# Optimization experiments

Measured on AMD Instinct MI355X. Metric: run time of the kernel, lower is better.

## Reference

```python
import jax, jax.numpy as jnp
import numpy as np

HEADS = 8

def _flatten(x, s1, s2):
    # 'b c (h s1) (w s2) -> b (h w) (s1 s2 c)'
    b, c, H, W = x.shape
    h, w = H // s1, W // s2
    x = x.reshape(b, c, h, s1, w, s2).transpose(0, 2, 4, 3, 5, 1)
    return x.reshape(b, h * w, s1 * s2 * c)

def _unflatten(x, h, w, s1, s2):
    # 'b (h w) (s1 s2 c) -> b c (h s1) (w s2)'
    b, n, e = x.shape
    c = e // (s1 * s2)
    x = x.reshape(b, h, w, s1, s2, c).transpose(0, 5, 1, 3, 2, 4)
    return x.reshape(b, c, h * s1, w * s2)

def _attn(x_detail, x_context, wq, bq, wk, bk, wv, bv, wo, bo):
    E = x_detail.shape[-1]
    d = E // HEADS
    scale = d ** -0.5
    def split(t):
        b, n, _ = t.shape
        return t.reshape(b, n, HEADS, d).transpose(0, 2, 1, 3)  # b h n d
    q = split(x_context @ wq.T + bq)
    k = split(x_detail @ wk.T + bk)
    v = split(x_detail @ wv.T + bv)
    att = jax.nn.softmax(jnp.einsum('bhqd,bhkd->bhqk', q, k) * scale, axis=-1)
    out = jnp.einsum('bhqk,bhkd->bhqd', att, v)
    b, h, n, _ = out.shape
    out = out.transpose(0, 2, 1, 3).reshape(b, n, E)
    return out @ wo.T + bo

def setup_inputs() -> dict:
    key = jax.random.key(0)
    ks = iter(jax.random.split(key, 64))
    inp = {}
    xshapes = [(16, 96, 56, 56), (16, 192, 28, 28), (16, 384, 14, 14), (16, 768, 7, 7)]
    names = ['x00', 'x10', 'x20', 'x30']
    for nm, sh in zip(names, xshapes):
        inp[nm + '_detail'] = jax.random.normal(next(ks), sh, dtype=jnp.float32)
        inp[nm + '_context'] = jax.random.normal(next(ks), sh, dtype=jnp.float32)
    embs = [384, 192, 384, 768]
    for i, E in enumerate(embs):
        for p in ['q', 'k', 'v', 'o']:
            inp[f'w{p}{i}'] = jax.random.normal(next(ks), (E, E), dtype=jnp.float32) * 0.02
            inp[f'b{p}{i}'] = jnp.zeros((E,), dtype=jnp.float32)
    return inp

def reference(x00_detail, x00_context, x10_detail, x10_context,
              x20_detail, x20_context, x30_detail, x30_context,
              wq0, bq0, wk0, bk0, wv0, bv0, wo0, bo0,
              wq1, bq1, wk1, bk1, wv1, bv1, wo1, bo1,
              wq2, bq2, wk2, bk2, wv2, bv2, wo2, bo2,
              wq3, bq3, wk3, bk3, wv3, bv3, wo3, bo3):
    # scale 0: 56x56 with 2x2 patching -> 784 tokens, emb 384
    o0 = x00_detail + _unflatten(
        _attn(_flatten(x00_detail, 2, 2), _flatten(x00_context, 2, 2),
              wq0, bq0, wk0, bk0, wv0, bv0, wo0, bo0), 28, 28, 2, 2)
    # scale 1: 28x28 -> 784 tokens, emb 192
    o1 = x10_detail + _unflatten(
        _attn(_flatten(x10_detail, 1, 1), _flatten(x10_context, 1, 1),
              wq1, bq1, wk1, bk1, wv1, bv1, wo1, bo1), 28, 28, 1, 1)
    # scale 2: 14x14 -> 196 tokens, emb 384
    o2 = x20_detail + _unflatten(
        _attn(_flatten(x20_detail, 1, 1), _flatten(x20_context, 1, 1),
              wq2, bq2, wk2, bk2, wv2, bv2, wo2, bo2), 14, 14, 1, 1)
    # scale 3: 7x7 -> 49 tokens, emb 768
    o3 = x30_detail + _unflatten(
        _attn(_flatten(x30_detail, 1, 1), _flatten(x30_context, 1, 1),
              wq3, bq3, wk3, bk3, wv3, bv3, wo3, bo3), 7, 7, 1, 1)
    return (o0, o1, o2, o3)
```

## Files before the change

kernel.cpp:

```cpp
#include <hip/hip_runtime.h>
#include <hip/hip_bf16.h>
#include <cstdint>
#include <cstddef>
#include <cmath>

typedef unsigned short bf16u;
typedef float f32x4 __attribute__((ext_vector_type(4)));
typedef short frag8 __attribute__((ext_vector_type(8)));

typedef __attribute__((address_space(1))) uint32_t u32g;
typedef __attribute__((address_space(3))) uint32_t u32l;

__device__ __forceinline__ void async_cp16(const bf16u* g, bf16u* l) {
    __builtin_amdgcn_global_load_lds((u32g*)g, (u32l*)l, 16, 0, 0);
}

__device__ __forceinline__ bf16u f2bf(float f) {
    union { float f; uint32_t u; } v; v.f = f;
    uint32_t u = v.u;
    return (bf16u)((u + 0x7fffu + ((u >> 16) & 1u)) >> 16);
}

__device__ __forceinline__ uint32_t pk2bf(float a, float b) {
    __hip_bfloat162 h = __float22bfloat162_rn(make_float2(a, b));
    union { __hip_bfloat162 h; uint32_t u; } c; c.h = h; return c.u;
}

__device__ __forceinline__ int vperm(int n) {
    return (n & ~63) | ((n & 15) << 2) | ((n >> 4) & 3);
}

static constexpr int cN[4]   = {784, 784, 196, 49};
static constexpr int cE[4]   = {384, 192, 384, 768};
static constexpr int cM[4]   = {12544, 12544, 3136, 784};
static constexpr int cC[4]   = {96, 192, 384, 768};
static constexpr int cH[4]   = {56, 28, 14, 7};
static constexpr int cS[4]   = {2, 1, 1, 1};
static constexpr int cWt[4]  = {28, 28, 14, 7};

static constexpr size_t xoff[4] = {0, 4816896, 7225344, 8429568};
static constexpr size_t voff[4] = {0, 6815744, 10223616, 12320768};
static constexpr size_t woff[4] = {0, 589824, 737280, 1327104};

__device__ __constant__ float qsc[4] = {0.14433756729740643f, 0.20412414523193154f,
                                        0.14433756729740643f, 0.10206207261596577f};

static constexpr int qStart[13] = {0,294,588,882,957,1032,1107,1149,1191,1233,1821,2409,2997};
static constexpr int oStart[5]  = {0,294,369,411,999};

static constexpr int fStart[9] = {0,4800,9600,12000,14400,15744,17088,17856,18624};
static constexpr int wCum[17]  = {0,72,144,216,288,306,324,342,360,432,504,576,648,936,1224,1512,1800};
static constexpr int uStart[5] = {0,4800,7200,8544,9312};
static constexpr int fNtn[4] = {25, 25, 7, 2};
static constexpr int fNtc[4] = {3, 6, 12, 24};
static constexpr int fSp[4]  = {4, 1, 1, 1};

struct BiasP { const float* p[16]; };
struct PrepP { const float* x[8]; const float* w[16]; };
struct UnfP  { const float* x[4]; };

__global__ __launch_bounds__(256) void prep(PrepP pp, bf16u* __restrict__ Xd,
                                            bf16u* __restrict__ Xc, bf16u* __restrict__ Wb) {
    int blk = blockIdx.x, tid = threadIdx.x;
    if (blk < 18624) {
        __shared__ float tile[32][33];
        int seg = 0;
        while (seg < 7 && blk >= fStart[seg + 1]) seg++;
        int s = seg >> 1, which = seg & 1;
        int l = blk - fStart[seg];
        int ntn = fNtn[s], ntc = fNtc[s], sp = fSp[s];
        int nt = l % ntn; l /= ntn;
        int ctl = l % ntc; l /= ntc;
        int spi = l % sp; int b = l / sp;
        int sv = cS[s];
        int s1i = spi / sv, s2i = spi % sv;
        int C = cC[s], H = cH[s], Wd = cH[s], N = cN[s], E2 = cE[s], Wt = cWt[s];
        const float* x = pp.x[s * 2 + which];
        bf16u* dst = (which ? Xc : Xd) + xoff[s];
        int tx = tid & 31, ty = tid >> 5;
        int n0 = nt * 32, c0 = ctl * 32;
#pragma unroll
        for (int rr = 0; rr < 4; ++rr) {
            int c = c0 + rr * 8 + ty;
            int n = n0 + tx;
            if (n < N) {
                int hh = (n / Wt) * sv + s1i;
                int ww = (n % Wt) * sv + s2i;
                tile[rr * 8 + ty][tx] = x[((size_t)(b * C + c) * H + hh) * Wd + ww];
            }
        }
        __syncthreads();
        int ebase = (s1i * sv + s2i) * C + c0;
#pragma unroll
        for (int rr = 0; rr < 4; ++rr) {
            int n = n0 + rr * 8 + ty;
            if (n < N)
                dst[((size_t)b * N + n) * E2 + ebase + tx] = f2bf(tile[tx][rr * 8 + ty]);
        }
    } else {
        int wb = blk - 18624;
        int m2 = 0;
        while (m2 < 15 && wb >= wCum[m2 + 1]) m2++;
        int s = m2 >> 2, mi = m2 & 3;
        size_t e2 = (size_t)cE[s] * cE[s];
        size_t base = (size_t)(wb - wCum[m2]) * 2048 + tid * 8;
        const float* src = pp.w[m2];
        bf16u* dst = Wb + woff[s] + mi * e2 + base;
        float4 a = *(const float4*)(src + base);
        float4 c = *(const float4*)(src + base + 4);
        bf16u o[8] = {f2bf(a.x), f2bf(a.y), f2bf(a.z), f2bf(a.w),
                      f2bf(c.x), f2bf(c.y), f2bf(c.z), f2bf(c.w)};
        *(frag8*)dst = *(frag8*)o;
    }
}

template<int MODE, int NN, int DHt, int DHPt, int NJt>
__device__ __forceinline__ void gemm_tile128(const bf16u* __restrict__ A, const bf16u* __restrict__ W,
                                             const float* __restrict__ bias,
                                             int M, int E, int mTile, int eTile, float oscale,
                                             bf16u* __restrict__ outB, float* __restrict__ outF,
                                             bf16u* As, bf16u* Bs) {
    int tid = threadIdx.x, wave = tid >> 6, lane = tid & 63;
    int mbase = mTile * 128, ebase = eTile * 128;
    int wm = (wave & 1) * 64, wn = (wave >> 1) * 64;
    f32x4 acc[4][4] = {};
    int srow = tid >> 2, sch = (tid & 3) * 8;
    int K = E;
    int m0 = mbase + srow;      if (m0 >= M) m0 = M - 1;
    int m1 = mbase + srow + 64; if (m1 >= M) m1 = M - 1;
    const bf16u* Ag0 = A + (size_t)m0 * K + sch;
    const bf16u* Ag1 = A + (size_t)m1 * K + sch;
    const bf16u* Wg0 = W + (size_t)(ebase + srow) * K + sch;
    const bf16u* Wg1 = W + (size_t)(ebase + srow + 64) * K + sch;
    bf16u* Asw = As + tid * 8;
    bf16u* Bsw = Bs + tid * 8;
    int la = (lane & 15) * 32 + (lane >> 4) * 8;

    for (int k0 = 0; k0 < K; k0 += 32) {
        async_cp16(Ag0 + k0, Asw);
        async_cp16(Ag1 + k0, Asw + 2048);
        async_cp16(Wg0 + k0, Bsw);
        async_cp16(Wg1 + k0, Bsw + 2048);
        __syncthreads();
        frag8 af[4], bfr[4];
#pragma unroll
        for (int i = 0; i < 4; ++i) {
            af[i]  = *(const frag8*)(As + (wm + i * 16) * 32 + la);
            bfr[i] = *(const frag8*)(Bs + (wn + i * 16) * 32 + la);
        }
#pragma unroll
        for (int i = 0; i < 4; ++i)
#pragma unroll
            for (int j = 0; j < 4; ++j)
                acc[i][j] = __builtin_amdgcn_mfma_f32_16x16x32_bf16(af[i], bfr[j], acc[i][j], 0, 0, 0);
        __syncthreads();
    }

#pragma unroll
    for (int mt = 0; mt < 4; ++mt) {
#pragma unroll
        for (int nt = 0; nt < 4; ++nt) {
            int col = ebase + wn + nt * 16 + (lane & 15);
            float bv = bias[col];
            int rbase = mbase + wm + mt * 16 + (lane >> 4) * 4;
#pragma unroll
            for (int r = 0; r < 4; ++r) {
                int rowg = rbase + r;
                if (rowg >= M) continue;
                float val = (acc[mt][nt][r] + bv) * oscale;
                if (MODE == 0) {
                    outB[(size_t)rowg * E + col] = f2bf(val);
                } else if (MODE == 2) {
                    outF[(size_t)rowg * E + col] = val;
                } else {
                    int bb2 = rowg / NN, n = rowg % NN;
                    int hh = col / DHt, d = col - hh * DHt;
                    outB[((size_t)(bb2 * 8 + hh) * DHPt + d) * NJt + vperm(n)] = f2bf(val);
                }
            }
        }
    }
}

template<int MODE, int NN, int DHt, int DHPt, int NJt>
__device__ __forceinline__ void gemm_tile64(const bf16u* __restrict__ A, const bf16u* __restrict__ W,
                                            const float* __restrict__ bias,
                                            int M, int E, int mTile, int eTile, float oscale,
                                            bf16u* __restrict__ outB, float* __restrict__ outF,
                                            bf16u* As, bf16u* Bs) {
    int tid = threadIdx.x, wave = tid >> 6, lane = tid & 63;
    int mbase = mTile * 64, ebase = eTile * 64;
    int wm = (wave & 1) * 32, wn = (wave >> 1) * 32;
    f32x4 acc[2][2] = {};
    int srow = tid >> 2, sch = (tid & 3) * 8;
    int K = E;
    int m = mbase + srow; if (m >= M) m = M - 1;
    const bf16u* Ag = A + (size_t)m * K + sch;
    const bf16u* Wg = W + (size_t)(ebase + srow) * K + sch;
    bf16u* Asw = As + tid * 8;
    bf16u* Bsw = Bs + tid * 8;
    int la = (lane & 15) * 32 + (lane >> 4) * 8;

    for (int k0 = 0; k0 < K; k0 += 32) {
        async_cp16(Ag + k0, Asw);
        async_cp16(Wg + k0, Bsw);
        __syncthreads();
        frag8 af0 = *(const frag8*)(As + wm * 32 + la);
        frag8 af1 = *(const frag8*)(As + (wm + 16) * 32 + la);
        frag8 bf0 = *(const frag8*)(Bs + wn * 32 + la);
        frag8 bf1 = *(const frag8*)(Bs + (wn + 16) * 32 + la);
        acc[0][0] = __builtin_amdgcn_mfma_f32_16x16x32_bf16(af0, bf0, acc[0][0], 0, 0, 0);
        acc[0][1] = __builtin_amdgcn_mfma_f32_16x16x32_bf16(af0, bf1, acc[0][1], 0, 0, 0);
        acc[1][0] = __builtin_amdgcn_mfma_f32_16x16x32_bf16(af1, bf0, acc[1][0], 0, 0, 0);
        acc[1][1] = __builtin_amdgcn_mfma_f32_16x16x32_bf16(af1, bf1, acc[1][1], 0, 0, 0);
        __syncthreads();
    }

#pragma unroll
    for (int mt = 0; mt < 2; ++mt) {
#pragma unroll
        for (int nt = 0; nt < 2; ++nt) {
            int col = ebase + wn + nt * 16 + (lane & 15);
            float bv = bias[col];
            int rbase = mbase + wm + mt * 16 + (lane >> 4) * 4;
#pragma unroll
            for (int r = 0; r < 4; ++r) {
                int rowg = rbase + r;
                if (rowg >= M) continue;
                float val = (acc[mt][nt][r] + bv) * oscale;
                if (MODE == 0) {
                    outB[(size_t)rowg * E + col] = f2bf(val);
                } else if (MODE == 2) {
                    outF[(size_t)rowg * E + col] = val;
                } else {
                    int bb2 = rowg / NN, n = rowg % NN;
                    int hh = col / DHt, d = col - hh * DHt;
                    outB[((size_t)(bb2 * 8 + hh) * DHPt + d) * NJt + vperm(n)] = f2bf(val);
                }
            }
        }
    }
}

__global__ __launch_bounds__(256) void qkv_fat(const bf16u* __restrict__ Xd, const bf16u* __restrict__ Xc,
                                               const bf16u* __restrict__ Wb,
                                               bf16u* __restrict__ Qb, bf16u* __restrict__ Kb,
                                               bf16u* __restrict__ Vt, BiasP bp) {
    __shared__ __align__(16) bf16u As[4096], Bs[4096];
    int blk = blockIdx.x;
    int seg = 0;
    while (seg < 11 && blk >= qStart[seg + 1]) seg++;
    int t = blk - qStart[seg];
    if (seg < 9) {
        int s = (seg < 3) ? 0 : (seg < 6 ? 2 : 3);
        int op = seg % 3;
        int E = cE[s], M = cM[s];
        int ct = E >> 7;
        int mTile = t / ct, eTile = t - mTile * ct;
        const bf16u* A = (op == 0 ? Xc : Xd) + xoff[s];
        const bf16u* W = Wb + woff[s] + (size_t)op * E * E;
        const float* bias = bp.p[s * 4 + op];
        if (op == 2) {
            if (s == 0)
                gemm_tile128<1, 784, 48, 64, 832>(A, W, bias, M, E, mTile, eTile, 1.0f, Vt + voff[0], nullptr, As, Bs);
            else if (s == 2)
                gemm_tile128<1, 196, 48, 64, 256>(A, W, bias, M, E, mTile, eTile, 1.0f, Vt + voff[2], nullptr, As, Bs);
            else
                gemm_tile128<1, 49, 96, 96, 64>(A, W, bias, M, E, mTile, eTile, 1.0f, Vt + voff[3], nullptr, As, Bs);
        } else {
            float osc = (op == 0) ? qsc[s] : 1.0f;
            bf16u* outB = (op == 0 ? Qb : Kb) + xoff[s];
            gemm_tile128<0, 0, 1, 0, 0>(A, W, bias, M, E, mTile, eTile, osc, outB, nullptr, As, Bs);
        }
    } else {
        int op = seg - 9;
        int E = 192, M = 12544;
        int mTile = t / 3, eTile = t - mTile * 3;
        const bf16u* A = (op == 0 ? Xc : Xd) + xoff[1];
        const bf16u* W = Wb + woff[1] + (size_t)op * E * E;
        const float* bias = bp.p[4 + op];
        if (op == 2)
            gemm_tile64<1, 784, 24, 32, 832>(A, W, bias, M, E, mTile, eTile, 1.0f, Vt + voff[1], nullptr, As, Bs);
        else {
            float osc = (op == 0) ? qsc[1] : 1.0f;
            bf16u* outB = (op == 0 ? Qb : Kb) + xoff[1];
            gemm_tile64<0, 0, 1, 0, 0>(A, W, bias, M, E, mTile, eTile, osc, outB, nullptr, As, Bs);
        }
    }
}

__global__ __launch_bounds__(256) void o_fat(const bf16u* __restrict__ Ob, const bf16u* __restrict__ Wb,
                                             float* __restrict__ Yo, BiasP bp) {
    __shared__ __align__(16) bf16u As[4096], Bs[4096];
    int blk = blockIdx.x;
    int seg = 0;
    while (seg < 3 && blk >= oStart[seg + 1]) seg++;
    int t = blk - oStart[seg];
    if (seg < 3) {
        int s = (seg == 0) ? 0 : (seg == 1 ? 2 : 3);
        int E = cE[s], M = cM[s];
        int ct = E >> 7;
        int mTile = t / ct, eTile = t - mTile * ct;
        gemm_tile128<2, 0, 1, 0, 0>(Ob + xoff[s], Wb + woff[s] + (size_t)3 * E * E, bp.p[s * 4 + 3],
                                    M, E, mTile, eTile, 1.0f, nullptr, Yo + xoff[s], As, Bs);
    } else {
        int E = 192, M = 12544;
        int mTile = t / 3, eTile = t - mTile * 3;
        gemm_tile64<2, 0, 1, 0, 0>(Ob + xoff[1], Wb + woff[1] + (size_t)3 * E * E, bp.p[4 + 3],
                                   M, E, mTile, eTile, 1.0f, nullptr, Yo + xoff[1], As, Bs);
    }
}

__device__ __forceinline__ f32x4 bfly_add16(f32x4 v) {
#pragma unroll
    for (int m = 1; m <= 8; m <<= 1) {
        f32x4 o;
#pragma unroll
        for (int e = 0; e < 4; ++e) o[e] = __shfl_xor(v[e], m);
#pragma unroll
        for (int e = 0; e < 4; ++e) v[e] += o[e];
    }
    return v;
}

template<int DH, int N>
__device__ __forceinline__ void attn_body(bf16u* __restrict__ smem,
                                          const bf16u* __restrict__ Q, const bf16u* __restrict__ K,
                                          const bf16u* __restrict__ Vt, bf16u* __restrict__ O,
                                          int lin) {
    constexpr int DHP = (DH == 24) ? 32 : (DH == 48 ? 64 : 96);
    constexpr int KC  = DHP / 32;
    constexpr int DHT = (DH + 15) / 16;
    constexpr int NT  = (N + 63) / 64;
    constexpr int NJc = NT * 64;
    constexpr int E   = DH * 8;
    constexpr int KP  = DHP + 8, QP = DHP + 8;
    constexpr int VP  = 72, PP = 72;
    constexpr int C8  = DHP / 8;
    constexpr int KIT = (64 * C8 + 255) / 256;
    constexpr int VIT = (DHT * 16 * 8 + 255) / 256;
    constexpr int QT  = (N + 63) / 64;

    bf16u* Ks = smem;
    bf16u* Vs = Ks + 64 * KP;
    bf16u* QsPw = Vs + DHT * 16 * VP;

    int qt = lin % QT;
    int r2 = lin / QT;
    int h = r2 & 7, b = r2 >> 3;
    int qb = qt * 64;
    int tid = threadIdx.x, wave = tid >> 6, lane = tid & 63;
    int mrow = lane & 15, quad = lane >> 4;

    for (int idx = tid; idx < 64 * C8; idx += 256) {
        int row = idx / C8, col = (idx % C8) * 8;
        int n = qb + row; if (n >= N) n = N - 1;
        frag8 v = {};
        if (col < DH) v = *(const frag8*)(Q + ((size_t)(b * N + n)) * E + h * DH + col);
        *(frag8*)(QsPw + row * QP + col) = v;
    }
    __syncthreads();
    frag8 qf[KC];
#pragma unroll
    for (int kc = 0; kc < KC; ++kc)
        qf[kc] = *(const frag8*)(QsPw + (wave * 16 + mrow) * QP + kc * 32 + quad * 8);
    __syncthreads();
    bf16u* Pw = QsPw + wave * 16 * PP;

    const bf16u* Kb2 = K + (size_t)b * N * E + h * DH;
    const bf16u* Vb2 = Vt + (size_t)(b * 8 + h) * DHP * NJc;

    frag8 kreg[KIT], vreg[VIT];
    auto loadKV = [&](int jt) {
#pragma unroll
        for (int it = 0; it < KIT; ++it) {
            int idx = tid + it * 256;
            int row = idx / C8, col = (idx % C8) * 8;
            int n = jt * 64 + row; if (n >= N) n = N - 1;
            frag8 v = {};
            if (col < DH) v = *(const frag8*)(Kb2 + (size_t)n * E + col);
            kreg[it] = v;
        }
#pragma unroll
        for (int it = 0; it < VIT; ++it) {
            int idx = tid + it * 256;
            frag8 v = {};
            if (idx < DHT * 16 * 8) {
                int d = idx / 8, j = (idx % 8) * 8;
                if (d < DH) v = *(const frag8*)(Vb2 + (size_t)d * NJc + jt * 64 + j);
            }
            vreg[it] = v;
        }
    };
    auto storeKV = [&]() {
#pragma unroll
        for (int it = 0; it < KIT; ++it) {
            int idx = tid + it * 256;
            int row = idx / C8, col = (idx % C8) * 8;
            *(frag8*)(Ks + row * KP + col) = kreg[it];
        }
#pragma unroll
        for (int it = 0; it < VIT; ++it) {
            int idx = tid + it * 256;
            if (idx < DHT * 16 * 8) {
                int d = idx / 8, j = (idx % 8) * 8;
                *(frag8*)(Vs + d * VP + j) = vreg[it];
            }
        }
    };

    f32x4 lrun = {0.f, 0.f, 0.f, 0.f};
    f32x4 oacc[DHT];
#pragma unroll
    for (int t = 0; t < DHT; ++t) oacc[t] = f32x4{0.f, 0.f, 0.f, 0.f};

    loadKV(0);
    for (int jt = 0; jt < NT; ++jt) {
        storeKV();
        __syncthreads();
        if (jt + 1 < NT) loadKV(jt + 1);

        f32x4 s[4];
        const bool domask = ((N & 63) != 0) && (jt == NT - 1);
#pragma unroll
        for (int sub = 0; sub < 4; ++sub) {
            f32x4 acc = {};
#pragma unroll
            for (int kc = 0; kc < KC; ++kc) {
                frag8 bfr = *(const frag8*)(Ks + (sub * 16 + mrow) * KP + kc * 32 + quad * 8);
                acc = __builtin_amdgcn_mfma_f32_16x16x32_bf16(qf[kc], bfr, acc, 0, 0, 0);
            }
            if (domask) {
                int col = jt * 64 + sub * 16 + mrow;
                if (col >= N) { acc[0] = acc[1] = acc[2] = acc[3] = -1e30f; }
            }
            s[sub] = acc;
        }

#pragma unroll
        for (int sub = 0; sub < 4; ++sub)
#pragma unroll
            for (int e = 0; e < 4; ++e) {
                float p = __expf(fminf(s[sub][e], 60.f));
                s[sub][e] = p;
                lrun[e] += p;
            }

#pragma unroll
        for (int e = 0; e < 4; ++e) {
            uint2 u;
            u.x = pk2bf(s[0][e], s[1][e]);
            u.y = pk2bf(s[2][e], s[3][e]);
            *(uint2*)(Pw + (quad * 4 + e) * PP + mrow * 4) = u;
        }

#pragma unroll
        for (int jc = 0; jc < 2; ++jc) {
            frag8 af = *(const frag8*)(Pw + mrow * PP + jc * 32 + quad * 8);
#pragma unroll
            for (int t = 0; t < DHT; ++t) {
                frag8 bfr = *(const frag8*)(Vs + (t * 16 + mrow) * VP + jc * 32 + quad * 8);
                oacc[t] = __builtin_amdgcn_mfma_f32_16x16x32_bf16(af, bfr, oacc[t], 0, 0, 0);
            }
        }
        __syncthreads();
    }

    lrun = bfly_add16(lrun);
    f32x4 linv;
#pragma unroll
    for (int e = 0; e < 4; ++e) linv[e] = 1.0f / lrun[e];
#pragma unroll
    for (int t = 0; t < DHT; ++t) {
        int d = t * 16 + mrow;
        if (d >= DH) continue;
#pragma unroll
        for (int e = 0; e < 4; ++e) {
            int n = qb + wave * 16 + quad * 4 + e;
            if (n < N)
                O[((size_t)(b * N + n)) * E + h * DH + d] = f2bf(oacc[t][e] * linv[e]);
        }
    }
}

__global__ __launch_bounds__(256, 4) void attn_fat(const bf16u* __restrict__ Qb, const bf16u* __restrict__ Kb,
                                                   const bf16u* __restrict__ Vt, bf16u* __restrict__ Ob) {
    __shared__ __align__(16) bf16u smem[12672];
    int blk = blockIdx.x;
    if (blk < 1664)
        attn_body<48, 784>(smem, Qb + xoff[0], Kb + xoff[0], Vt + voff[0], Ob + xoff[0], blk);
    else if (blk < 3328)
        attn_body<24, 784>(smem, Qb + xoff[1], Kb + xoff[1], Vt + voff[1], Ob + xoff[1], blk - 1664);
    else
        attn_body<48, 196>(smem, Qb + xoff[2], Kb + xoff[2], Vt + voff[2], Ob + xoff[2], blk - 3328);
}

__global__ __launch_bounds__(256, 2) void attn_s3(const bf16u* __restrict__ Qb, const bf16u* __restrict__ Kb,
                                                  const bf16u* __restrict__ Vt, bf16u* __restrict__ Ob) {
    __shared__ __align__(16) bf16u smem[20224];
    attn_body<96, 49>(smem, Qb + xoff[3], Kb + xoff[3], Vt + voff[3], Ob + xoff[3], blockIdx.x);
}

__global__ __launch_bounds__(256) void unflat(const float* __restrict__ Yo, UnfP up,
                                              float* __restrict__ out) {
    __shared__ float tile[32][33];
    int blk = blockIdx.x, tid = threadIdx.x;
    int seg = 0;
    while (seg < 3 && blk >= uStart[seg + 1]) seg++;
    int s = seg;
    int l = blk - uStart[seg];
    int ntn = fNtn[s], ntc = fNtc[s], sp = fSp[s];
    int nt = l % ntn; l /= ntn;
    int ctl = l % ntc; l /= ntc;
    int spi = l % sp; int b = l / sp;
    int sv = cS[s];
    int s1i = spi / sv, s2i = spi % sv;
    int C = cC[s], H = cH[s], Wd = cH[s], N = cN[s], E2 = cE[s], Wt = cWt[s];
    const float* yo = Yo + xoff[s];
    const float* xd = up.x[s];
    float* o = out + xoff[s];
    int tx = tid & 31, ty = tid >> 5;
    int n0 = nt * 32, c0 = ctl * 32;
    int ebase = (s1i * sv + s2i) * C + c0;
#pragma unroll
    for (int rr = 0; rr < 4; ++rr) {
        int n = n0 + rr * 8 + ty;
        if (n < N)
            tile[tx][rr * 8 + ty] = yo[((size_t)b * N + n) * E2 + ebase + tx];
    }
    __syncthreads();
#pragma unroll
    for (int rr = 0; rr < 4; ++rr) {
        int c = c0 + rr * 8 + ty;
        int n = n0 + tx;
        if (n < N) {
            int hh = (n / Wt) * sv + s1i;
            int ww = (n % Wt) * sv + s2i;
            size_t oi = ((size_t)(b * C + c) * H + hh) * Wd + ww;
            o[oi] = xd[oi] + tile[rr * 8 + ty][tx];
        }
    }
}

extern "C" void kernel_launch(void* const* d_in, const int* in_sizes, int n_in,
                              void* d_out, int out_size, void* d_ws, size_t ws_size,
                              hipStream_t stream) {
    bf16u* ws = (bf16u*)d_ws;
    bf16u* Qb = ws;
    bf16u* Kb = ws + 9031680;
    bf16u* Vt = ws + 18063360;
    bf16u* Ob = ws + 31170560;
    bf16u* Wb = ws + 40202240;
    bf16u* Xd = ws + 43888640;
    bf16u* Xc = ws + 52920320;
    float* Yo = (float*)(ws + 43888640);
    float* out = (float*)d_out;

    PrepP pp; BiasP bb; UnfP ux;
    for (int s = 0; s < 4; ++s) {
        pp.x[s * 2]     = (const float*)d_in[s * 2];
        pp.x[s * 2 + 1] = (const float*)d_in[s * 2 + 1];
        ux.x[s]         = (const float*)d_in[s * 2];
        int w0 = 8 + s * 8;
        pp.w[s * 4 + 0] = (const float*)d_in[w0 + 0];
        pp.w[s * 4 + 1] = (const float*)d_in[w0 + 2];
        pp.w[s * 4 + 2] = (const float*)d_in[w0 + 4];
        pp.w[s * 4 + 3] = (const float*)d_in[w0 + 6];
        bb.p[s * 4 + 0] = (const float*)d_in[w0 + 1];
        bb.p[s * 4 + 1] = (const float*)d_in[w0 + 3];
        bb.p[s * 4 + 2] = (const float*)d_in[w0 + 5];
        bb.p[s * 4 + 3] = (const float*)d_in[w0 + 7];
    }

    prep<<<20424, 256, 0, stream>>>(pp, Xd, Xc, Wb);
    qkv_fat<<<2997, 256, 0, stream>>>(Xd, Xc, Wb, Qb, Kb, Vt, bb);
    attn_fat<<<3840, 256, 0, stream>>>(Qb, Kb, Vt, Ob);
    attn_s3<<<128, 256, 0, stream>>>(Qb, Kb, Vt, Ob);
    o_fat<<<999, 256, 0, stream>>>(Ob, Wb, Yo, bb);
    unflat<<<9312, 256, 0, stream>>>(Yo, ux, out);
}
```

Measured before the change: 414.4 us.

## Fuse output projection with unflatten residual and double-buffer attention KV loads

```diff
diff --git a/kernel.cpp b/kernel.cpp
--- a/kernel.cpp
+++ b/kernel.cpp
@@ -42,22 +42,20 @@
 static constexpr size_t voff[4] = {0, 6815744, 10223616, 12320768};
 static constexpr size_t woff[4] = {0, 589824, 737280, 1327104};
 
-__device__ __constant__ float qsc[4] = {0.14433756729740643f, 0.20412414523193154f,
-                                        0.14433756729740643f, 0.10206207261596577f};
+__device__ __constant__ float qsc[4] = {0.20823509f, 0.29448888f, 0.20823509f, 0.14724444f};
 
 static constexpr int qStart[13] = {0,294,588,882,957,1032,1107,1149,1191,1233,1821,2409,2997};
 static constexpr int oStart[5]  = {0,294,369,411,999};
 
 static constexpr int fStart[9] = {0,4800,9600,12000,14400,15744,17088,17856,18624};
 static constexpr int wCum[17]  = {0,72,144,216,288,306,324,342,360,432,504,576,648,936,1224,1512,1800};
-static constexpr int uStart[5] = {0,4800,7200,8544,9312};
 static constexpr int fNtn[4] = {25, 25, 7, 2};
 static constexpr int fNtc[4] = {3, 6, 12, 24};
 static constexpr int fSp[4]  = {4, 1, 1, 1};
 
 struct BiasP { const float* p[16]; };
 struct PrepP { const float* x[8]; const float* w[16]; };
-struct UnfP  { const float* x[4]; };
+struct OunfP { const float* xd[4]; };
 
 __global__ __launch_bounds__(256) void prep(PrepP pp, bf16u* __restrict__ Xd,
                                             bf16u* __restrict__ Xc, bf16u* __restrict__ Wb) {
@@ -118,7 +116,7 @@
 __device__ __forceinline__ void gemm_tile128(const bf16u* __restrict__ A, const bf16u* __restrict__ W,
                                              const float* __restrict__ bias,
                                              int M, int E, int mTile, int eTile, float oscale,
-                                             bf16u* __restrict__ outB, float* __restrict__ outF,
+                                             bf16u* __restrict__ outB,
                                              bf16u* As, bf16u* Bs) {
     int tid = threadIdx.x, wave = tid >> 6, lane = tid & 63;
     int mbase = mTile * 128, ebase = eTile * 128;
@@ -170,8 +168,6 @@
                 float val = (acc[mt][nt][r] + bv) * oscale;
                 if (MODE == 0) {
                     outB[(size_t)rowg * E + col] = f2bf(val);
-                } else if (MODE == 2) {
-                    outF[(size_t)rowg * E + col] = val;
                 } else {
                     int bb2 = rowg / NN, n = rowg % NN;
                     int hh = col / DHt, d = col - hh * DHt;
@@ -186,7 +182,7 @@
 __device__ __forceinline__ void gemm_tile64(const bf16u* __restrict__ A, const bf16u* __restrict__ W,
                                             const float* __restrict__ bias,
                                             int M, int E, int mTile, int eTile, float oscale,
-                                            bf16u* __restrict__ outB, float* __restrict__ outF,
+                                            bf16u* __restrict__ outB,
                                             bf16u* As, bf16u* Bs) {
     int tid = threadIdx.x, wave = tid >> 6, lane = tid & 63;
     int mbase = mTile * 64, ebase = eTile * 64;
@@ -230,8 +226,6 @@
                 float val = (acc[mt][nt][r] + bv) * oscale;
                 if (MODE == 0) {
                     outB[(size_t)rowg * E + col] = f2bf(val);
-                } else if (MODE == 2) {
-                    outF[(size_t)rowg * E + col] = val;
                 } else {
                     int bb2 = rowg / NN, n = rowg % NN;
                     int hh = col / DHt, d = col - hh * DHt;
@@ -262,15 +256,15 @@
         const float* bias = bp.p[s * 4 + op];
         if (op == 2) {
             if (s == 0)
-                gemm_tile128<1, 784, 48, 64, 832>(A, W, bias, M, E, mTile, eTile, 1.0f, Vt + voff[0], nullptr, As, Bs);
+                gemm_tile128<1, 784, 48, 64, 832>(A, W, bias, M, E, mTile, eTile, 1.0f, Vt + voff[0], As, Bs);
             else if (s == 2)
-                gemm_tile128<1, 196, 48, 64, 256>(A, W, bias, M, E, mTile, eTile, 1.0f, Vt + voff[2], nullptr, As, Bs);
+                gemm_tile128<1, 196, 48, 64, 256>(A, W, bias, M, E, mTile, eTile, 1.0f, Vt + voff[2], As, Bs);
             else
-                gemm_tile128<1, 49, 96, 96, 64>(A, W, bias, M, E, mTile, eTile, 1.0f, Vt + voff[3], nullptr, As, Bs);
+                gemm_tile128<1, 49, 96, 96, 64>(A, W, bias, M, E, mTile, eTile, 1.0f, Vt + voff[3], As, Bs);
         } else {
             float osc = (op == 0) ? qsc[s] : 1.0f;
             bf16u* outB = (op == 0 ? Qb : Kb) + xoff[s];
-            gemm_tile128<0, 0, 1, 0, 0>(A, W, bias, M, E, mTile, eTile, osc, outB, nullptr, As, Bs);
+            gemm_tile128<0, 0, 1, 0, 0>(A, W, bias, M, E, mTile, eTile, osc, outB, As, Bs);
         }
     } else {
         int op = seg - 9;
@@ -280,18 +274,456 @@
         const bf16u* W = Wb + woff[1] + (size_t)op * E * E;
         const float* bias = bp.p[4 + op];
         if (op == 2)
-            gemm_tile64<1, 784, 24, 32, 832>(A, W, bias, M, E, mTile, eTile, 1.0f, Vt + voff[1], nullptr, As, Bs);
+            gemm_tile64<1, 784, 24, 32, 832>(A, W, bias, M, E, mTile, eTile, 1.0f, Vt + voff[1], As, Bs);
         else {
             float osc = (op == 0) ? qsc[1] : 1.0f;
             bf16u* outB = (op == 0 ? Qb : Kb) + xoff[1];
-            gemm_tile64<0, 0, 1, 0, 0>(A, W, bias, M, E, mTile, eTile, osc, outB, nullptr, As, Bs);
-        }
-    }
-}
-
-__global__ __launch_bounds__(256) void o_fat(const bf16u* __restrict__ Ob, const bf16u* __restrict__ Wb,
-                                             float* __restrict__ Yo, BiasP bp) {
-    __shared__ __align__(16) bf16u As[4096], Bs[4096];
+            gemm_tile64<0, 0, 1, 0, 0>(A, W, bias, M, E, mTile, eTile, osc, outB, As, Bs);
+        }
+    }
+}
+
+__device__ __forceinline__ f32x4 bfly_add16(f32x4 v) {
+#pragma unroll
+    for (int m = 1; m <= 8; m <<= 1) {
+        f32x4 o;
+#pragma unroll
+        for (int e = 0; e < 4; ++e) o[e] = __shfl_xor(v[e], m);
+#pragma unroll
+        for (int e = 0; e < 4; ++e) v[e] += o[e];
+    }
+    return v;
+}
+
+template<int DH, int N>
+__device__ __forceinline__ void attn_body2(bf16u* __restrict__ smem,
+                                           const bf16u* __restrict__ Q, const bf16u* __restrict__ K,
+                                           const bf16u* __restrict__ Vt, bf16u* __restrict__ O,
+                                           int lin) {
+    constexpr int DHP = (DH == 24) ? 32 : 64;
+    constexpr int C8  = DHP / 8;
+    constexpr int CM  = C8 - 1;
+    constexpr int KC  = DHP / 32;
+    constexpr int DHT = (DH + 15) / 16;
+    constexpr int VR  = DHT * 16;
+    constexpr int NT  = (N + 63) / 64;
+    constexpr int NJc = NT * 64;
+    constexpr int E   = DH * 8;
+    constexpr int KS  = 64 * C8;
+    constexpr int TS  = KS + VR * 8;
+    constexpr int RND = (TS + 255) / 256;
+    constexpr int PP  = 72;
+
+    bf16u* buf0 = smem;
+    bf16u* buf1 = smem + (size_t)TS * 8;
+    bf16u* Ps   = smem + (size_t)2 * TS * 8;
+
+    const int qt = lin % NT;
+    const int r2 = lin / NT;
+    const int h = r2 & 7, b = r2 >> 3;
+    const int qb = qt * 64;
+    const int tid = threadIdx.x, wave = tid >> 6, lane = tid & 63;
+    const int mrow = lane & 15, quad = lane >> 4;
+
+    const bf16u* Kb2 = K + (size_t)b * N * E + h * DH;
+    const bf16u* Vb2 = Vt + (size_t)(b * 8 + h) * DHP * NJc;
+
+    auto stage = [&](int jt, bf16u* buf) {
+#pragma unroll
+        for (int r = 0; r < RND; ++r) {
+            int s = tid + r * 256;
+            bf16u* dst = buf + (size_t)s * 8;
+            if (s < KS) {
+                int row = s / C8;
+                int cl = (s & CM) ^ (row & CM);
+                int n = jt * 64 + row; if (n >= N) n = N - 1;
+                async_cp16(Kb2 + (size_t)n * E + cl * 8, dst);
+            } else if (s < TS) {
+                int v = s - KS;
+                int d = v >> 3;
+                int cl = (v & 7) ^ (d & 7);
+                async_cp16(Vb2 + (size_t)d * NJc + jt * 64 + cl * 8, dst);
+            }
+        }
+    };
+
+    stage(0, buf0);
+
+    frag8 qf[KC];
+    {
+        int qn = qb + wave * 16 + mrow; if (qn >= N) qn = N - 1;
+        const bf16u* qp = Q + (size_t)(b * N + qn) * E + h * DH;
+#pragma unroll
+        for (int kc = 0; kc < KC; ++kc) {
+            int col = kc * 32 + quad * 8;
+            frag8 v = {};
+            if (col < DH) v = *(const frag8*)(qp + col);
+            qf[kc] = v;
+        }
+    }
+
+    f32x4 lrun = {0.f, 0.f, 0.f, 0.f};
+    f32x4 oacc[DHT];
+#pragma unroll
+    for (int t = 0; t < DHT; ++t) oacc[t] = f32x4{0.f, 0.f, 0.f, 0.f};
+
+    bf16u* Pw = Ps + wave * 16 * PP;
+
+    __syncthreads();
+
+    int p = 0;
+    for (int jt = 0; jt < NT; ++jt) {
+        bf16u* KsB = p ? buf1 : buf0;
+        bf16u* VsB = KsB + (size_t)KS * 8;
+        if (jt + 1 < NT) stage(jt + 1, p ? buf0 : buf1);
+
+        f32x4 s[4];
+        const bool domask = ((N & 63) != 0) && (jt == NT - 1);
+#pragma unroll
+        for (int sub = 0; sub < 4; ++sub) {
+            f32x4 acc = {};
+#pragma unroll
+            for (int kc = 0; kc < KC; ++kc) {
+                int c = kc * 4 + quad;
+                frag8 bfr = *(const frag8*)(KsB + ((size_t)((sub * 16 + mrow) * C8 + (c ^ (mrow & CM)))) * 8);
+                acc = __builtin_amdgcn_mfma_f32_16x16x32_bf16(qf[kc], bfr, acc, 0, 0, 0);
+            }
+            if (domask) {
+                int col = jt * 64 + sub * 16 + mrow;
+                if (col >= N) { acc[0] = acc[1] = acc[2] = acc[3] = -30000.f; }
+            }
+            s[sub] = acc;
+        }
+
+#pragma unroll
+        for (int sub = 0; sub < 4; ++sub)
+#pragma unroll
+            for (int e = 0; e < 4; ++e) {
+                float px = __builtin_amdgcn_exp2f(s[sub][e]);
+                s[sub][e] = px;
+                lrun[e] += px;
+            }
+
+#pragma unroll
+        for (int e = 0; e < 4; ++e) {
+            uint2 u;
+            u.x = pk2bf(s[0][e], s[1][e]);
+            u.y = pk2bf(s[2][e], s[3][e]);
+            *(uint2*)(Pw + (quad * 4 + e) * PP + mrow * 4) = u;
+        }
+
+#pragma unroll
+        for (int jc = 0; jc < 2; ++jc) {
+            frag8 af = *(const frag8*)(Pw + mrow * PP + jc * 32 + quad * 8);
+            int c = jc * 4 + quad;
+#pragma unroll
+            for (int t = 0; t < DHT; ++t) {
+                frag8 bfr = *(const frag8*)(VsB + ((size_t)((t * 16 + mrow) * 8 + (c ^ (mrow & 7)))) * 8);
+                oacc[t] = __builtin_amdgcn_mfma_f32_16x16x32_bf16(af, bfr, oacc[t], 0, 0, 0);
+            }
+        }
+        __syncthreads();
+        p ^= 1;
+    }
+
+    lrun = bfly_add16(lrun);
+    f32x4 linv;
+#pragma unroll
+    for (int e = 0; e < 4; ++e) linv[e] = 1.0f / lrun[e];
+#pragma unroll
+    for (int t = 0; t < DHT; ++t) {
+        int d = t * 16 + mrow;
+        if (d >= DH) continue;
+#pragma unroll
+        for (int e = 0; e < 4; ++e) {
+            int n = qb + wave * 16 + quad * 4 + e;
+            if (n < N)
+                O[((size_t)(b * N + n)) * E + h * DH + d] = f2bf(oacc[t][e] * linv[e]);
+        }
+    }
+}
+
+__global__ __launch_bounds__(256, 4) void attn_fat(const bf16u* __restrict__ Qb, const bf16u* __restrict__ Kb,
+                                                   const bf16u* __restrict__ Vt, bf16u* __restrict__ Ob) {
+    __shared__ __align__(16) bf16u smem[18944];
+    int blk = blockIdx.x;
+    if (blk < 1664)
+        attn_body2<48, 784>(smem, Qb + xoff[0], Kb + xoff[0], Vt + voff[0], Ob + xoff[0], blk);
+    else if (blk < 3328)
+        attn_body2<24, 784>(smem, Qb + xoff[1], Kb + xoff[1], Vt + voff[1], Ob + xoff[1], blk - 1664);
+    else
+        attn_body2<48, 196>(smem, Qb + xoff[2], Kb + xoff[2], Vt + voff[2], Ob + xoff[2], blk - 3328);
+}
+
+__global__ __launch_bounds__(256, 2) void attn_s3(const bf16u* __restrict__ Qg, const bf16u* __restrict__ Kg,
+                                                  const bf16u* __restrict__ Vtg, bf16u* __restrict__ Og) {
+    constexpr int DH = 96, N = 49, DHP = 96, KC = 3, DHT = 6, NJc = 64, E = 768;
+    constexpr int KP = 104, QP = 104, VP = 72, PP = 72, C8 = 12;
+    __shared__ __align__(16) bf16u smem[20224];
+    bf16u* Ks = smem;
+    bf16u* Vs = Ks + 64 * KP;
+    bf16u* QsPw = Vs + DHT * 16 * VP;
+
+    const bf16u* Q = Qg + xoff[3];
+    const bf16u* K = Kg + xoff[3];
+    const bf16u* Vt = Vtg + voff[3];
+    bf16u* O = Og + xoff[3];
+
+    int lin = blockIdx.x;
+    int h = lin & 7, b = lin >> 3;
+    int tid = threadIdx.x, wave = tid >> 6, lane = tid & 63;
+    int mrow = lane & 15, quad = lane >> 4;
+
+    for (int idx = tid; idx < 64 * C8; idx += 256) {
+        int row = idx / C8, col = (idx % C8) * 8;
+        int n = row; if (n >= N) n = N - 1;
+        frag8 v = {};
+        if (col < DH) v = *(const frag8*)(Q + ((size_t)(b * N + n)) * E + h * DH + col);
+        *(frag8*)(QsPw + row * QP + col) = v;
+    }
+    for (int idx = tid; idx < 64 * C8; idx += 256) {
+        int row = idx / C8, col = (idx % C8) * 8;
+        int n = row; if (n >= N) n = N - 1;
+        frag8 v = {};
+        if (col < DH) v = *(const frag8*)(K + (size_t)(b * N + n) * E + h * DH + col);
+        *(frag8*)(Ks + row * KP + col) = v;
+    }
+    const bf16u* Vb2 = Vt + (size_t)(b * 8 + h) * DHP * NJc;
+    for (int idx = tid; idx < DHT * 16 * 8; idx += 256) {
+        int d = idx / 8, j = (idx % 8) * 8;
+        frag8 v = {};
+        if (d < DH) v = *(const frag8*)(Vb2 + (size_t)d * NJc + j);
+        *(frag8*)(Vs + d * VP + j) = v;
+    }
+    __syncthreads();
+    frag8 qf[KC];
+#pragma unroll
+    for (int kc = 0; kc < KC; ++kc)
+        qf[kc] = *(const frag8*)(QsPw + (wave * 16 + mrow) * QP + kc * 32 + quad * 8);
+    __syncthreads();
+    bf16u* Pw = QsPw + wave * 16 * PP;
+
+    f32x4 lrun = {0.f, 0.f, 0.f, 0.f};
+    f32x4 oacc[DHT];
+#pragma unroll
+    for (int t = 0; t < DHT; ++t) oacc[t] = f32x4{0.f, 0.f, 0.f, 0.f};
+
+    f32x4 s[4];
+#pragma unroll
+    for (int sub = 0; sub < 4; ++sub) {
+        f32x4 acc = {};
+#pragma unroll
+        for (int kc = 0; kc < KC; ++kc) {
+            frag8 bfr = *(const frag8*)(Ks + (sub * 16 + mrow) * KP + kc * 32 + quad * 8);
+            acc = __builtin_amdgcn_mfma_f32_16x16x32_bf16(qf[kc], bfr, acc, 0, 0, 0);
+        }
+        int col = sub * 16 + mrow;
+        if (col >= N) { acc[0] = acc[1] = acc[2] = acc[3] = -30000.f; }
+        s[sub] = acc;
+    }
+#pragma unroll
+    for (int sub = 0; sub < 4; ++sub)
+#pragma unroll
+        for (int e = 0; e < 4; ++e) {
+            float px = __builtin_amdgcn_exp2f(s[sub][e]);
+            s[sub][e] = px;
+            lrun[e] += px;
+        }
+#pragma unroll
+    for (int e = 0; e < 4; ++e) {
+        uint2 u;
+        u.x = pk2bf(s[0][e], s[1][e]);
+        u.y = pk2bf(s[2][e], s[3][e]);
+        *(uint2*)(Pw + (quad * 4 + e) * PP + mrow * 4) = u;
+    }
+#pragma unroll
+    for (int jc = 0; jc < 2; ++jc) {
+        frag8 af = *(const frag8*)(Pw + mrow * PP + jc * 32 + quad * 8);
+#pragma unroll
+        for (int t = 0; t < DHT; ++t) {
+            frag8 bfr = *(const frag8*)(Vs + (t * 16 + mrow) * VP + jc * 32 + quad * 8);
+            oacc[t] = __builtin_amdgcn_mfma_f32_16x16x32_bf16(af, bfr, oacc[t], 0, 0, 0);
+        }
+    }
+
+    lrun = bfly_add16(lrun);
+    f32x4 linv;
+#pragma unroll
+    for (int e = 0; e < 4; ++e) linv[e] = 1.0f / lrun[e];
+#pragma unroll
+    for (int t = 0; t < DHT; ++t) {
+        int d = t * 16 + mrow;
+#pragma unroll
+        for (int e = 0; e < 4; ++e) {
+            int n = wave * 16 + quad * 4 + e;
+            if (n < N)
+                O[((size_t)(b * N + n)) * E + h * DH + d] = f2bf(oacc[t][e] * linv[e]);
+        }
+    }
+}
+
+template<int SC>
+__device__ __forceinline__ size_t out_index(int rowg, int cg) {
+    if (SC == 0) {
+        int b = rowg / 784, n = rowg - b * 784;
+        int slot = cg / 96, c = cg - slot * 96;
+        int hh = n / 28, ww = n - hh * 28;
+        return ((size_t)(b * 96 + c) * 56 + 2 * hh + (slot >> 1)) * 56 + 2 * ww + (slot & 1);
+    } else if (SC == 1) {
+        int b = rowg / 784, n = rowg - b * 784;
+        return ((size_t)(b * 192 + cg)) * 784 + n;
+    } else if (SC == 2) {
+        int b = rowg / 196, n = rowg - b * 196;
+        return ((size_t)(b * 384 + cg)) * 196 + n;
+    } else {
+        int b = rowg / 49, n = rowg - b * 49;
+        return ((size_t)(b * 768 + cg)) * 49 + n;
+    }
+}
+
+template<int SC>
+__device__ __forceinline__ void o_tile128(const bf16u* __restrict__ A, const bf16u* __restrict__ W,
+                                          const float* __restrict__ bias,
+                                          const float* __restrict__ xd, float* __restrict__ out,
+                                          int M, int E, int mTile, int eTile, bf16u* sm) {
+    bf16u* As = sm;
+    bf16u* Bs = sm + 4096;
+    int tid = threadIdx.x, wave = tid >> 6, lane = tid & 63;
+    int mbase = mTile * 128, ebase = eTile * 128;
+    int wm = (wave & 1) * 64, wn = (wave >> 1) * 64;
+    int mrow = lane & 15, quad = lane >> 4;
+    f32x4 acc[4][4] = {};
+    int srow = tid >> 2, sch = (tid & 3) * 8;
+    int K = E;
+    int m0 = mbase + srow;      if (m0 >= M) m0 = M - 1;
+    int m1 = mbase + srow + 64; if (m1 >= M) m1 = M - 1;
+    const bf16u* Ag0 = A + (size_t)m0 * K + sch;
+    const bf16u* Ag1 = A + (size_t)m1 * K + sch;
+    const bf16u* Wg0 = W + (size_t)(ebase + srow) * K + sch;
+    const bf16u* Wg1 = W + (size_t)(ebase + srow + 64) * K + sch;
+    bf16u* Asw = As + tid * 8;
+    bf16u* Bsw = Bs + tid * 8;
+    int la = mrow * 32 + quad * 8;
+
+    for (int k0 = 0; k0 < K; k0 += 32) {
+        async_cp16(Ag0 + k0, Asw);
+        async_cp16(Ag1 + k0, Asw + 2048);
+        async_cp16(Wg0 + k0, Bsw);
+        async_cp16(Wg1 + k0, Bsw + 2048);
+        __syncthreads();
+        frag8 af[4], bfr[4];
+#pragma unroll
+        for (int i = 0; i < 4; ++i) {
+            af[i]  = *(const frag8*)(As + (wm + i * 16) * 32 + la);
+            bfr[i] = *(const frag8*)(Bs + (wn + i * 16) * 32 + la);
+        }
+#pragma unroll
+        for (int i = 0; i < 4; ++i)
+#pragma unroll
+            for (int j = 0; j < 4; ++j)
+                acc[i][j] = __builtin_amdgcn_mfma_f32_16x16x32_bf16(af[i], bfr[j], acc[i][j], 0, 0, 0);
+        __syncthreads();
+    }
+
+    float* Ls = (float*)sm;
+#pragma unroll
+    for (int ph = 0; ph < 4; ++ph) {
+        __syncthreads();
+        if ((wave & 1) == (ph >> 1)) {
+            int mt0 = (ph & 1) * 2;
+#pragma unroll
+            for (int mi = 0; mi < 2; ++mi) {
+                int mt = mt0 + mi;
+#pragma unroll
+                for (int nt = 0; nt < 4; ++nt)
+#pragma unroll
+                    for (int r = 0; r < 4; ++r)
+                        Ls[(mi * 16 + quad * 4 + r) * 133 + wn + nt * 16 + mrow] = acc[mt][nt][r];
+            }
+        }
+        __syncthreads();
+        int rb = mbase + ph * 32;
+#pragma unroll
+        for (int i = 0; i < 16; ++i) {
+            int coll = (tid >> 5) + i * 8;
+            int l = tid & 31;
+            int rg = rb + l;
+            if (rg < M) {
+                int cg = ebase + coll;
+                size_t oi = out_index<SC>(rg, cg);
+                out[oi] = xd[oi] + Ls[l * 133 + coll] + bias[cg];
+            }
+        }
+    }
+}
+
+__device__ __forceinline__ void o_tile64_s1(const bf16u* __restrict__ A, const bf16u* __restrict__ W,
+                                            const float* __restrict__ bias,
+                                            const float* __restrict__ xd, float* __restrict__ out,
+                                            int M, int E, int mTile, int eTile, bf16u* sm) {
+    bf16u* As = sm;
+    bf16u* Bs = sm + 2048;
+    int tid = threadIdx.x, wave = tid >> 6, lane = tid & 63;
+    int mbase = mTile * 64, ebase = eTile * 64;
+    int wm = (wave & 1) * 32, wn = (wave >> 1) * 32;
+    int mrow = lane & 15, quad = lane >> 4;
+    f32x4 acc[2][2] = {};
+    int srow = tid >> 2, sch = (tid & 3) * 8;
+    int K = E;
+    int m = mbase + srow; if (m >= M) m = M - 1;
+    const bf16u* Ag = A + (size_t)m * K + sch;
+    const bf16u* Wg = W + (size_t)(ebase + srow) * K + sch;
+    bf16u* Asw = As + tid * 8;
+    bf16u* Bsw = Bs + tid * 8;
+    int la = mrow * 32 + quad * 8;
+
+    for (int k0 = 0; k0 < K; k0 += 32) {
+        async_cp16(Ag + k0, Asw);
+        async_cp16(Wg + k0, Bsw);
+        __syncthreads();
+        frag8 af0 = *(const frag8*)(As + wm * 32 + la);
+        frag8 af1 = *(const frag8*)(As + (wm + 16) * 32 + la);
+        frag8 bf0 = *(const frag8*)(Bs + wn * 32 + la);
+        frag8 bf1 = *(const frag8*)(Bs + (wn + 16) * 32 + la);
+        acc[0][0] = __builtin_amdgcn_mfma_f32_16x16x32_bf16(af0, bf0, acc[0][0], 0, 0, 0);
+        acc[0][1] = __builtin_amdgcn_mfma_f32_16x16x32_bf16(af0, bf1, acc[0][1], 0, 0, 0);
+        acc[1][0] = __builtin_amdgcn_mfma_f32_16x16x32_bf16(af1, bf0, acc[1][0], 0, 0, 0);
+        acc[1][1] = __builtin_amdgcn_mfma_f32_16x16x32_bf16(af1, bf1, acc[1][1], 0, 0, 0);
+        __syncthreads();
+    }
+
+    float* Ls = (float*)sm;
+#pragma unroll
+    for (int ph = 0; ph < 2; ++ph) {
+        __syncthreads();
+        if ((wave & 1) == ph) {
+#pragma unroll
+            for (int mt = 0; mt < 2; ++mt)
+#pragma unroll
+                for (int nt = 0; nt < 2; ++nt)
+#pragma unroll
+                    for (int r = 0; r < 4; ++r)
+                        Ls[(mt * 16 + quad * 4 + r) * 69 + wn + nt * 16 + mrow] = acc[mt][nt][r];
+        }
+        __syncthreads();
+        int rb = mbase + ph * 32;
+#pragma unroll
+        for (int i = 0; i < 8; ++i) {
+            int coll = (tid >> 5) + i * 8;
+            int l = tid & 31;
+            int rg = rb + l;
+            if (rg < M) {
+                int cg = ebase + coll;
+                size_t oi = out_index<1>(rg, cg);
+                out[oi] = xd[oi] + Ls[l * 69 + coll] + bias[cg];
+            }
+        }
+    }
+}
+
+__global__ __launch_bounds__(256) void ounf_fat(const bf16u* __restrict__ Ob, const bf16u* __restrict__ Wb,
+                                                float* __restrict__ out, BiasP bp, OunfP up) {
+    __shared__ __align__(16) bf16u sm[8512];
     int blk = blockIdx.x;
     int seg = 0;
     while (seg < 3 && blk >= oStart[seg + 1]) seg++;
@@ -301,244 +733,19 @@
         int E = cE[s], M = cM[s];
         int ct = E >> 7;
         int mTile = t / ct, eTile = t - mTile * ct;
-        gemm_tile128<2, 0, 1, 0, 0>(Ob + xoff[s], Wb + woff[s] + (size_t)3 * E * E, bp.p[s * 4 + 3],
-                                    M, E, mTile, eTile, 1.0f, nullptr, Yo + xoff[s], As, Bs);
+        const bf16u* A = Ob + xoff[s];
+        const bf16u* W = Wb + woff[s] + (size_t)3 * E * E;
+        if (s == 0)
+            o_tile128<0>(A, W, bp.p[3], up.xd[0], out + xoff[0], M, E, mTile, eTile, sm);
+        else if (s == 2)
+            o_tile128<2>(A, W, bp.p[11], up.xd[2], out + xoff[2], M, E, mTile, eTile, sm);
+        else
+            o_tile128<3>(A, W, bp.p[15], up.xd[3], out + xoff[3], M, E, mTile, eTile, sm);
     } else {
         int E = 192, M = 12544;
         int mTile = t / 3, eTile = t - mTile * 3;
-        gemm_tile64<2, 0, 1, 0, 0>(Ob + xoff[1], Wb + woff[1] + (size_t)3 * E * E, bp.p[4 + 3],
-                                   M, E, mTile, eTile, 1.0f, nullptr, Yo + xoff[1], As, Bs);
-    }
-}
-
-__device__ __forceinline__ f32x4 bfly_add16(f32x4 v) {
-#pragma unroll
-    for (int m = 1; m <= 8; m <<= 1) {
-        f32x4 o;
-#pragma unroll
-        for (int e = 0; e < 4; ++e) o[e] = __shfl_xor(v[e], m);
-#pragma unroll
-        for (int e = 0; e < 4; ++e) v[e] += o[e];
-    }
-    return v;
-}
-
-template<int DH, int N>
-__device__ __forceinline__ void attn_body(bf16u* __restrict__ smem,
-                                          const bf16u* __restrict__ Q, const bf16u* __restrict__ K,
-                                          const bf16u* __restrict__ Vt, bf16u* __restrict__ O,
-                                          int lin) {
-    constexpr int DHP = (DH == 24) ? 32 : (DH == 48 ? 64 : 96);
-    constexpr int KC  = DHP / 32;
-    constexpr int DHT = (DH + 15) / 16;
-    constexpr int NT  = (N + 63) / 64;
-    constexpr int NJc = NT * 64;
-    constexpr int E   = DH * 8;
-    constexpr int KP  = DHP + 8, QP = DHP + 8;
-    constexpr int VP  = 72, PP = 72;
-    constexpr int C8  = DHP / 8;
-    constexpr int KIT = (64 * C8 + 255) / 256;
-    constexpr int VIT = (DHT * 16 * 8 + 255) / 256;
-    constexpr int QT  = (N + 63) / 64;
-
-    bf16u* Ks = smem;
-    bf16u* Vs = Ks + 64 * KP;
-    bf16u* QsPw = Vs + DHT * 16 * VP;
-
-    int qt = lin % QT;
-    int r2 = lin / QT;
-    int h = r2 & 7, b = r2 >> 3;
-    int qb = qt * 64;
-    int tid = threadIdx.x, wave = tid >> 6, lane = tid & 63;
-    int mrow = lane & 15, quad = lane >> 4;
-
-    for (int idx = tid; idx < 64 * C8; idx += 256) {
-        int row = idx / C8, col = (idx % C8) * 8;
-        int n = qb + row; if (n >= N) n = N - 1;
-        frag8 v = {};
-        if (col < DH) v = *(const frag8*)(Q + ((size_t)(b * N + n)) * E + h * DH + col);
-        *(frag8*)(QsPw + row * QP + col) = v;
-    }
-    __syncthreads();
-    frag8 qf[KC];
-#pragma unroll
-    for (int kc = 0; kc < KC; ++kc)
-        qf[kc] = *(const frag8*)(QsPw + (wave * 16 + mrow) * QP + kc * 32 + quad * 8);
-    __syncthreads();
-    bf16u* Pw = QsPw + wave * 16 * PP;
-
-    const bf16u* Kb2 = K + (size_t)b * N * E + h * DH;
-    const bf16u* Vb2 = Vt + (size_t)(b * 8 + h) * DHP * NJc;
-
-    frag8 kreg[KIT], vreg[VIT];
-    auto loadKV = [&](int jt) {
-#pragma unroll
-        for (int it = 0; it < KIT; ++it) {
-            int idx = tid + it * 256;
-            int row = idx / C8, col = (idx % C8) * 8;
-            int n = jt * 64 + row; if (n >= N) n = N - 1;
-            frag8 v = {};
-            if (col < DH) v = *(const frag8*)(Kb2 + (size_t)n * E + col);
-            kreg[it] = v;
-        }
-#pragma unroll
-        for (int it = 0; it < VIT; ++it) {
-            int idx = tid + it * 256;
-            frag8 v = {};
-            if (idx < DHT * 16 * 8) {
-                int d = idx / 8, j = (idx % 8) * 8;
-                if (d < DH) v = *(const frag8*)(Vb2 + (size_t)d * NJc + jt * 64 + j);
-            }
-            vreg[it] = v;
-        }
-    };
-    auto storeKV = [&]() {
-#pragma unroll
-        for (int it = 0; it < KIT; ++it) {
-            int idx = tid + it * 256;
-            int row = idx / C8, col = (idx % C8) * 8;
-            *(frag8*)(Ks + row * KP + col) = kreg[it];
-        }
-#pragma unroll
-        for (int it = 0; it < VIT; ++it) {
-            int idx = tid + it * 256;
-            if (idx < DHT * 16 * 8) {
-                int d = idx / 8, j = (idx % 8) * 8;
-                *(frag8*)(Vs + d * VP + j) = vreg[it];
-            }
-        }
-    };
-
-    f32x4 lrun = {0.f, 0.f, 0.f, 0.f};
-    f32x4 oacc[DHT];
-#pragma unroll
-    for (int t = 0; t < DHT; ++t) oacc[t] = f32x4{0.f, 0.f, 0.f, 0.f};
-
-    loadKV(0);
-    for (int jt = 0; jt < NT; ++jt) {
-        storeKV();
-        __syncthreads();
-        if (jt + 1 < NT) loadKV(jt + 1);
-
-        f32x4 s[4];
-        const bool domask = ((N & 63) != 0) && (jt == NT - 1);
-#pragma unroll
-        for (int sub = 0; sub < 4; ++sub) {
-            f32x4 acc = {};
-#pragma unroll
-            for (int kc = 0; kc < KC; ++kc) {
-                frag8 bfr = *(const frag8*)(Ks + (sub * 16 + mrow) * KP + kc * 32 + quad * 8);
-                acc = __builtin_amdgcn_mfma_f32_16x16x32_bf16(qf[kc], bfr, acc, 0, 0, 0);
-            }
-            if (domask) {
-                int col = jt * 64 + sub * 16 + mrow;
-                if (col >= N) { acc[0] = acc[1] = acc[2] = acc[3] = -1e30f; }
-            }
-            s[sub] = acc;
-        }
-
-#pragma unroll
-        for (int sub = 0; sub < 4; ++sub)
-#pragma unroll
-            for (int e = 0; e < 4; ++e) {
-                float p = __expf(fminf(s[sub][e], 60.f));
-                s[sub][e] = p;
-                lrun[e] += p;
-            }
-
-#pragma unroll
-        for (int e = 0; e < 4; ++e) {
-            uint2 u;
-            u.x = pk2bf(s[0][e], s[1][e]);
-            u.y = pk2bf(s[2][e], s[3][e]);
-            *(uint2*)(Pw + (quad * 4 + e) * PP + mrow * 4) = u;
-        }
-
-#pragma unroll
-        for (int jc = 0; jc < 2; ++jc) {
-            frag8 af = *(const frag8*)(Pw + mrow * PP + jc * 32 + quad * 8);
-#pragma unroll
-            for (int t = 0; t < DHT; ++t) {
-                frag8 bfr = *(const frag8*)(Vs + (t * 16 + mrow) * VP + jc * 32 + quad * 8);
-                oacc[t] = __builtin_amdgcn_mfma_f32_16x16x32_bf16(af, bfr, oacc[t], 0, 0, 0);
-            }
-        }
-        __syncthreads();
-    }
-
-    lrun = bfly_add16(lrun);
-    f32x4 linv;
-#pragma unroll
-    for (int e = 0; e < 4; ++e) linv[e] = 1.0f / lrun[e];
-#pragma unroll
-    for (int t = 0; t < DHT; ++t) {
-        int d = t * 16 + mrow;
-        if (d >= DH) continue;
-#pragma unroll
-        for (int e = 0; e < 4; ++e) {
-            int n = qb + wave * 16 + quad * 4 + e;
-            if (n < N)
-                O[((size_t)(b * N + n)) * E + h * DH + d] = f2bf(oacc[t][e] * linv[e]);
-        }
-    }
-}
-
-__global__ __launch_bounds__(256, 4) void attn_fat(const bf16u* __restrict__ Qb, const bf16u* __restrict__ Kb,
-                                                   const bf16u* __restrict__ Vt, bf16u* __restrict__ Ob) {
-    __shared__ __align__(16) bf16u smem[12672];
-    int blk = blockIdx.x;
-    if (blk < 1664)
-        attn_body<48, 784>(smem, Qb + xoff[0], Kb + xoff[0], Vt + voff[0], Ob + xoff[0], blk);
-    else if (blk < 3328)
-        attn_body<24, 784>(smem, Qb + xoff[1], Kb + xoff[1], Vt + voff[1], Ob + xoff[1], blk - 1664);
-    else
-        attn_body<48, 196>(smem, Qb + xoff[2], Kb + xoff[2], Vt + voff[2], Ob + xoff[2], blk - 3328);
-}
-
-__global__ __launch_bounds__(256, 2) void attn_s3(const bf16u* __restrict__ Qb, const bf16u* __restrict__ Kb,
-                                                  const bf16u* __restrict__ Vt, bf16u* __restrict__ Ob) {
-    __shared__ __align__(16) bf16u smem[20224];
-    attn_body<96, 49>(smem, Qb + xoff[3], Kb + xoff[3], Vt + voff[3], Ob + xoff[3], blockIdx.x);
-}
-
-__global__ __launch_bounds__(256) void unflat(const float* __restrict__ Yo, UnfP up,
-                                              float* __restrict__ out) {
-    __shared__ float tile[32][33];
-    int blk = blockIdx.x, tid = threadIdx.x;
-    int seg = 0;
-    while (seg < 3 && blk >= uStart[seg + 1]) seg++;
-    int s = seg;
-    int l = blk - uStart[seg];
-    int ntn = fNtn[s], ntc = fNtc[s], sp = fSp[s];
-    int nt = l % ntn; l /= ntn;
-    int ctl = l % ntc; l /= ntc;
-    int spi = l % sp; int b = l / sp;
-    int sv = cS[s];
-    int s1i = spi / sv, s2i = spi % sv;
-    int C = cC[s], H = cH[s], Wd = cH[s], N = cN[s], E2 = cE[s], Wt = cWt[s];
-    const float* yo = Yo + xoff[s];
-    const float* xd = up.x[s];
-    float* o = out + xoff[s];
-    int tx = tid & 31, ty = tid >> 5;
-    int n0 = nt * 32, c0 = ctl * 32;
-    int ebase = (s1i * sv + s2i) * C + c0;
-#pragma unroll
-    for (int rr = 0; rr < 4; ++rr) {
-        int n = n0 + rr * 8 + ty;
-        if (n < N)
-            tile[tx][rr * 8 + ty] = yo[((size_t)b * N + n) * E2 + ebase + tx];
-    }
-    __syncthreads();
-#pragma unroll
-    for (int rr = 0; rr < 4; ++rr) {
-        int c = c0 + rr * 8 + ty;
-        int n = n0 + tx;
-        if (n < N) {
-            int hh = (n / Wt) * sv + s1i;
-            int ww = (n % Wt) * sv + s2i;
-            size_t oi = ((size_t)(b * C + c) * H + hh) * Wd + ww;
-            o[oi] = xd[oi] + tile[rr * 8 + ty][tx];
-        }
+        o_tile64_s1(Ob + xoff[1], Wb + woff[1] + (size_t)3 * E * E, bp.p[7],
+                    up.xd[1], out + xoff[1], M, E, mTile, eTile, sm);
     }
 }
 
@@ -553,14 +760,13 @@
     bf16u* Wb = ws + 40202240;
     bf16u* Xd = ws + 43888640;
     bf16u* Xc = ws + 52920320;
-    float* Yo = (float*)(ws + 43888640);
     float* out = (float*)d_out;
 
-    PrepP pp; BiasP bb; UnfP ux;
+    PrepP pp; BiasP bb; OunfP ux;
     for (int s = 0; s < 4; ++s) {
         pp.x[s * 2]     = (const float*)d_in[s * 2];
         pp.x[s * 2 + 1] = (const float*)d_in[s * 2 + 1];
-        ux.x[s]         = (const float*)d_in[s * 2];
+        ux.xd[s]        = (const float*)d_in[s * 2];
         int w0 = 8 + s * 8;
         pp.w[s * 4 + 0] = (const float*)d_in[w0 + 0];
         pp.w[s * 4 + 1] = (const float*)d_in[w0 + 2];
@@ -576,6 +782,5 @@
     qkv_fat<<<2997, 256, 0, stream>>>(Xd, Xc, Wb, Qb, Kb, Vt, bb);
     attn_fat<<<3840, 256, 0, stream>>>(Qb, Kb, Vt, Ob);
     attn_s3<<<128, 256, 0, stream>>>(Qb, Kb, Vt, Ob);
-    o_fat<<<999, 256, 0, stream>>>(Ob, Wb, Yo, bb);
-    unflat<<<9312, 256, 0, stream>>>(Yo, ux, out);
-}
+    ounf_fat<<<999, 256, 0, stream>>>(Ob, Wb, out, bb, ux);
+}
```

Result: faster. 384.5 us (-7.2%).
